# Kernel optimization log

Hardware: AMD Instinct MI355X
Metric: run time of the kernel (lower is better)

The kernel has to match this reference:

```python
import jax, jax.numpy as jnp
import numpy as np

N = 1_000_000
C = 128
B = 16  # number of instances (batch segments)
EPS = 1e-5


def setup_inputs() -> dict:
    key = jax.random.key(0)
    k1, k2 = jax.random.split(key)
    x = jax.random.normal(k1, (N, C), dtype=jnp.float32)
    batch_idx = jnp.sort(jax.random.randint(k2, (N,), 0, B, dtype=jnp.int32))
    weight = jnp.ones((1, C), dtype=jnp.float32)
    bias = jnp.zeros((1, C), dtype=jnp.float32)
    return {"x": x, "batch_idx": batch_idx, "weight": weight, "bias": bias}


def reference(x, batch_idx, weight, bias):
    # per-instance counts [B, 1]
    cnt = jax.ops.segment_sum(jnp.ones((x.shape[0], 1), x.dtype), batch_idx,
                              num_segments=B)
    cnt = jnp.maximum(cnt, 1.0)
    # segment mean [B, C]
    mean = jax.ops.segment_sum(x, batch_idx, num_segments=B) / cnt
    centered = x - mean[batch_idx]               # broadcast-add of -mean
    # segment mean of squared centered features -> per-instance variance [B, C]
    var = jax.ops.segment_sum(centered * centered, batch_idx, num_segments=B) / cnt
    instd = 1.0 / jnp.sqrt(var + EPS)            # [B, C]
    # broadcast-multiply, then affine
    return centered * instd[batch_idx] * weight + bias
```

## Files before the change

### kernel.cpp

```cpp
#include <hip/hip_runtime.h>

#define CC 128
#define BSEG 16
#define EPSV 1e-5f
#define ROWS_PER_BLOCK 512

typedef float v4f __attribute__((ext_vector_type(4)));

__global__ __launch_bounds__(256) void ms_stats(const float* __restrict__ x,
                                                const int* __restrict__ bidx,
                                                int n,
                                                float* __restrict__ sum,
                                                float* __restrict__ sumsq,
                                                float* __restrict__ cnt)
{
    const int r0 = blockIdx.x * ROWS_PER_BLOCK;
    if (r0 >= n) return;
    const int rend = min(r0 + ROWS_PER_BLOCK, n);
    const int tq = threadIdx.x & 31;
    const int tr = threadIdx.x >> 5;

    const int seg_first = bidx[r0];
    const int seg_last  = bidx[rend - 1];

    float s0 = 0.f, s1 = 0.f, s2 = 0.f, s3 = 0.f;
    float q0 = 0.f, q1 = 0.f, q2 = 0.f, q3 = 0.f;

    if (seg_first == seg_last) {
        for (int r = r0 + tr; r < rend; r += 8) {
            const v4f v = *reinterpret_cast<const v4f*>(x + (size_t)r * CC + tq * 4);
            s0 += v.x; s1 += v.y; s2 += v.z; s3 += v.w;
            q0 += v.x * v.x; q1 += v.y * v.y; q2 += v.z * v.z; q3 += v.w * v.w;
        }
        __shared__ float red[8][8][32];
        red[tr][0][tq] = s0; red[tr][1][tq] = s1; red[tr][2][tq] = s2; red[tr][3][tq] = s3;
        red[tr][4][tq] = q0; red[tr][5][tq] = q1; red[tr][6][tq] = q2; red[tr][7][tq] = q3;
        __syncthreads();
        const int j = threadIdx.x >> 5;
        float acc = 0.f;
        #pragma unroll
        for (int k = 0; k < 8; ++k) acc += red[k][j][tq];
        const int ch = tq * 4 + (j & 3);
        atomicAdd(((j < 4) ? sum : sumsq) + seg_first * CC + ch, acc);
        if (threadIdx.x == 0)
            atomicAdd(cnt + seg_first, (float)(rend - r0));
    } else {
        int cur = -1;
        float rows = 0.f;
        for (int r = r0 + tr; r < rend; r += 8) {
            const int seg = bidx[r];
            if (seg != cur) {
                if (cur >= 0) {
                    float* sd = sum   + cur * CC + tq * 4;
                    float* qd = sumsq + cur * CC + tq * 4;
                    atomicAdd(sd + 0, s0); atomicAdd(sd + 1, s1);
                    atomicAdd(sd + 2, s2); atomicAdd(sd + 3, s3);
                    atomicAdd(qd + 0, q0); atomicAdd(qd + 1, q1);
                    atomicAdd(qd + 2, q2); atomicAdd(qd + 3, q3);
                    if (tq == 0) atomicAdd(cnt + cur, rows);
                    s0 = s1 = s2 = s3 = q0 = q1 = q2 = q3 = 0.f;
                    rows = 0.f;
                }
                cur = seg;
            }
            const v4f v = *reinterpret_cast<const v4f*>(x + (size_t)r * CC + tq * 4);
            s0 += v.x; s1 += v.y; s2 += v.z; s3 += v.w;
            q0 += v.x * v.x; q1 += v.y * v.y; q2 += v.z * v.z; q3 += v.w * v.w;
            rows += 1.f;
        }
        if (cur >= 0) {
            float* sd = sum   + cur * CC + tq * 4;
            float* qd = sumsq + cur * CC + tq * 4;
            atomicAdd(sd + 0, s0); atomicAdd(sd + 1, s1);
            atomicAdd(sd + 2, s2); atomicAdd(sd + 3, s3);
            atomicAdd(qd + 0, q0); atomicAdd(qd + 1, q1);
            atomicAdd(qd + 2, q2); atomicAdd(qd + 3, q3);
            if (tq == 0) atomicAdd(cnt + cur, rows);
        }
    }
}

__global__ __launch_bounds__(256) void ms_norm(const float* __restrict__ x,
                                               const int* __restrict__ bidx,
                                               const float* __restrict__ sum,
                                               const float* __restrict__ sumsq,
                                               const float* __restrict__ cnt,
                                               const float* __restrict__ w,
                                               const float* __restrict__ bias,
                                               float* __restrict__ out,
                                               int n)
{
    __shared__ float s_scale[BSEG * CC];
    __shared__ float s_shift[BSEG * CC];
    for (int i = threadIdx.x; i < BSEG * CC; i += 256) {
        const int b = i >> 7;
        const int c = i & (CC - 1);
        const float nn   = fmaxf(cnt[b], 1.0f);
        const float mean = sum[i] / nn;
        const float var  = fmaxf(sumsq[i] / nn - mean * mean, 0.0f);
        const float sc   = rsqrtf(var + EPSV) * w[c];
        s_scale[i] = sc;
        s_shift[i] = fmaf(-mean, sc, bias[c]);
    }
    __syncthreads();

    const unsigned total  = (unsigned)n * 32u;
    const unsigned stride = gridDim.x * blockDim.x;
    for (unsigned i = blockIdx.x * blockDim.x + threadIdx.x; i < total; i += stride) {
        const unsigned idx = total - 1u - i;
        const int r = (int)(idx >> 5);
        const int q = (int)(idx & 31);
        const int seg  = bidx[r];
        const int base = seg * CC + q * 4;
        const v4f v = reinterpret_cast<const v4f*>(x)[idx];
        v4f o;
        o.x = fmaf(v.x, s_scale[base + 0], s_shift[base + 0]);
        o.y = fmaf(v.y, s_scale[base + 1], s_shift[base + 1]);
        o.z = fmaf(v.z, s_scale[base + 2], s_shift[base + 2]);
        o.w = fmaf(v.w, s_scale[base + 3], s_shift[base + 3]);
        __builtin_nontemporal_store(o, reinterpret_cast<v4f*>(out) + idx);
    }
}

extern "C" void kernel_launch(void* const* d_in, const int* in_sizes, int n_in,
                              void* d_out, int out_size, void* d_ws, size_t ws_size,
                              hipStream_t stream)
{
    const float* x    = (const float*)d_in[0];
    const int*   bidx = (const int*)d_in[1];
    const float* w    = (const float*)d_in[2];
    const float* bias = (const float*)d_in[3];
    float* out = (float*)d_out;
    const int n = in_sizes[1];

    float* ws    = (float*)d_ws;
    float* sum   = ws;
    float* sumsq = ws + BSEG * CC;
    float* cnt   = ws + 2 * BSEG * CC;

    (void)hipMemsetAsync(d_ws, 0, (size_t)(2 * BSEG * CC + BSEG) * sizeof(float), stream);

    const int g1 = (n + ROWS_PER_BLOCK - 1) / ROWS_PER_BLOCK;
    ms_stats<<<g1, 256, 0, stream>>>(x, bidx, n, sum, sumsq, cnt);
    ms_norm<<<2048, 256, 0, stream>>>(x, bidx, sum, sumsq, cnt, w, bias, out, n);
}
```

Measured before the change: 316.5 us.

## Process segments in groups so normalize re-reads x from cache

The stats and normalize passes are split into four per-group launches, each covering four consecutive segments (about a quarter of x). The normalize pass re-reads a group's rows soon after the stats pass, so those rows can come from the last-level cache rather than HBM. Segment boundaries are found by binary search on the sorted batch index. That replaces the per-row bidx loads and the count atomics, and the per-row segment lookup becomes comparisons against the boundaries. In exchange there are eight kernel launches instead of two, and the 2048 blocks per launch may be underused on small groups.

```diff
diff --git a/kernel.cpp b/kernel.cpp
--- a/kernel.cpp
+++ b/kernel.cpp
@@ -2,32 +2,52 @@
 
 #define CC 128
 #define BSEG 16
+#define GRP 4
+#define NGRP (BSEG / GRP)
 #define EPSV 1e-5f
-#define ROWS_PER_BLOCK 512
 
 typedef float v4f __attribute__((ext_vector_type(4)));
 
-__global__ __launch_bounds__(256) void ms_stats(const float* __restrict__ x,
-                                                const int* __restrict__ bidx,
-                                                int n,
-                                                float* __restrict__ sum,
-                                                float* __restrict__ sumsq,
-                                                float* __restrict__ cnt)
+__device__ __forceinline__ int lower_bound_dev(const int* __restrict__ a, int n, int v)
 {
-    const int r0 = blockIdx.x * ROWS_PER_BLOCK;
-    if (r0 >= n) return;
-    const int rend = min(r0 + ROWS_PER_BLOCK, n);
+    int lo = 0, hi = n;
+    while (lo < hi) {
+        const int mid = (lo + hi) >> 1;
+        if (a[mid] < v) lo = mid + 1; else hi = mid;
+    }
+    return lo;
+}
+
+__global__ __launch_bounds__(256) void ms_stats_g(const float* __restrict__ x,
+                                                  const int* __restrict__ bidx, int n,
+                                                  float* __restrict__ sum,
+                                                  float* __restrict__ sumsq,
+                                                  int g)
+{
+    __shared__ int sb[GRP + 1];
+    if (threadIdx.x <= GRP)
+        sb[threadIdx.x] = lower_bound_dev(bidx, n, g * GRP + (int)threadIdx.x);
+    __syncthreads();
+    const int b0 = sb[0], b1 = sb[1], b2 = sb[2], b3 = sb[3], b4 = sb[4];
+
+    const int R = b4 - b0;
+    if (R <= 0) return;
+    const int chunk = (R + gridDim.x - 1) / gridDim.x;
+    const int rs = b0 + blockIdx.x * chunk;
+    const int re = min(rs + chunk, b4);
+    if (rs >= re) return;
+
     const int tq = threadIdx.x & 31;
     const int tr = threadIdx.x >> 5;
-
-    const int seg_first = bidx[r0];
-    const int seg_last  = bidx[rend - 1];
 
     float s0 = 0.f, s1 = 0.f, s2 = 0.f, s3 = 0.f;
     float q0 = 0.f, q1 = 0.f, q2 = 0.f, q3 = 0.f;
 
-    if (seg_first == seg_last) {
-        for (int r = r0 + tr; r < rend; r += 8) {
+    const int segA = (rs >= b1) + (rs >= b2) + (rs >= b3);
+    const int segB = ((re - 1) >= b1) + ((re - 1) >= b2) + ((re - 1) >= b3);
+
+    if (segA == segB) {
+        for (int r = rs + tr; r < re; r += 8) {
             const v4f v = *reinterpret_cast<const v4f*>(x + (size_t)r * CC + tq * 4);
             s0 += v.x; s1 += v.y; s2 += v.z; s3 += v.w;
             q0 += v.x * v.x; q1 += v.y * v.y; q2 += v.z * v.z; q3 += v.w * v.w;
@@ -41,83 +61,83 @@
         #pragma unroll
         for (int k = 0; k < 8; ++k) acc += red[k][j][tq];
         const int ch = tq * 4 + (j & 3);
-        atomicAdd(((j < 4) ? sum : sumsq) + seg_first * CC + ch, acc);
-        if (threadIdx.x == 0)
-            atomicAdd(cnt + seg_first, (float)(rend - r0));
+        atomicAdd(((j < 4) ? sum : sumsq) + (g * GRP + segA) * CC + ch, acc);
     } else {
         int cur = -1;
-        float rows = 0.f;
-        for (int r = r0 + tr; r < rend; r += 8) {
-            const int seg = bidx[r];
+        for (int r = rs + tr; r < re; r += 8) {
+            const int seg = (r >= b1) + (r >= b2) + (r >= b3);
             if (seg != cur) {
                 if (cur >= 0) {
-                    float* sd = sum   + cur * CC + tq * 4;
-                    float* qd = sumsq + cur * CC + tq * 4;
+                    float* sd = sum   + (g * GRP + cur) * CC + tq * 4;
+                    float* qd = sumsq + (g * GRP + cur) * CC + tq * 4;
                     atomicAdd(sd + 0, s0); atomicAdd(sd + 1, s1);
                     atomicAdd(sd + 2, s2); atomicAdd(sd + 3, s3);
                     atomicAdd(qd + 0, q0); atomicAdd(qd + 1, q1);
                     atomicAdd(qd + 2, q2); atomicAdd(qd + 3, q3);
-                    if (tq == 0) atomicAdd(cnt + cur, rows);
                     s0 = s1 = s2 = s3 = q0 = q1 = q2 = q3 = 0.f;
-                    rows = 0.f;
                 }
                 cur = seg;
             }
             const v4f v = *reinterpret_cast<const v4f*>(x + (size_t)r * CC + tq * 4);
             s0 += v.x; s1 += v.y; s2 += v.z; s3 += v.w;
             q0 += v.x * v.x; q1 += v.y * v.y; q2 += v.z * v.z; q3 += v.w * v.w;
-            rows += 1.f;
         }
         if (cur >= 0) {
-            float* sd = sum   + cur * CC + tq * 4;
-            float* qd = sumsq + cur * CC + tq * 4;
+            float* sd = sum   + (g * GRP + cur) * CC + tq * 4;
+            float* qd = sumsq + (g * GRP + cur) * CC + tq * 4;
             atomicAdd(sd + 0, s0); atomicAdd(sd + 1, s1);
             atomicAdd(sd + 2, s2); atomicAdd(sd + 3, s3);
             atomicAdd(qd + 0, q0); atomicAdd(qd + 1, q1);
             atomicAdd(qd + 2, q2); atomicAdd(qd + 3, q3);
-            if (tq == 0) atomicAdd(cnt + cur, rows);
         }
     }
 }
 
-__global__ __launch_bounds__(256) void ms_norm(const float* __restrict__ x,
-                                               const int* __restrict__ bidx,
-                                               const float* __restrict__ sum,
-                                               const float* __restrict__ sumsq,
-                                               const float* __restrict__ cnt,
-                                               const float* __restrict__ w,
-                                               const float* __restrict__ bias,
-                                               float* __restrict__ out,
-                                               int n)
+__global__ __launch_bounds__(256) void ms_norm_g(const float* __restrict__ x,
+                                                 const int* __restrict__ bidx, int n,
+                                                 const float* __restrict__ sum,
+                                                 const float* __restrict__ sumsq,
+                                                 const float* __restrict__ w,
+                                                 const float* __restrict__ bias,
+                                                 float* __restrict__ out,
+                                                 int g)
 {
-    __shared__ float s_scale[BSEG * CC];
-    __shared__ float s_shift[BSEG * CC];
-    for (int i = threadIdx.x; i < BSEG * CC; i += 256) {
-        const int b = i >> 7;
-        const int c = i & (CC - 1);
-        const float nn   = fmaxf(cnt[b], 1.0f);
-        const float mean = sum[i] / nn;
-        const float var  = fmaxf(sumsq[i] / nn - mean * mean, 0.0f);
+    __shared__ int sb[GRP + 1];
+    __shared__ v4f s_scale[GRP * 32];
+    __shared__ v4f s_shift[GRP * 32];
+    if (threadIdx.x <= GRP)
+        sb[threadIdx.x] = lower_bound_dev(bidx, n, g * GRP + (int)threadIdx.x);
+    __syncthreads();
+
+    for (int i = threadIdx.x; i < GRP * CC; i += 256) {
+        const int sl = i >> 7;
+        const int c  = i & (CC - 1);
+        const float nn   = fmaxf((float)(sb[sl + 1] - sb[sl]), 1.0f);
+        const int   gi   = (g * GRP + sl) * CC + c;
+        const float mean = sum[gi] / nn;
+        const float var  = fmaxf(sumsq[gi] / nn - mean * mean, 0.0f);
         const float sc   = rsqrtf(var + EPSV) * w[c];
-        s_scale[i] = sc;
-        s_shift[i] = fmaf(-mean, sc, bias[c]);
+        reinterpret_cast<float*>(s_scale)[i] = sc;
+        reinterpret_cast<float*>(s_shift)[i] = fmaf(-mean, sc, bias[c]);
     }
     __syncthreads();
+    const int b1 = sb[1], b2 = sb[2], b3 = sb[3];
 
-    const unsigned total  = (unsigned)n * 32u;
+    const unsigned f0 = (unsigned)sb[0] * 32u;
+    const unsigned f4 = (unsigned)sb[4] * 32u;
     const unsigned stride = gridDim.x * blockDim.x;
-    for (unsigned i = blockIdx.x * blockDim.x + threadIdx.x; i < total; i += stride) {
-        const unsigned idx = total - 1u - i;
-        const int r = (int)(idx >> 5);
-        const int q = (int)(idx & 31);
-        const int seg  = bidx[r];
-        const int base = seg * CC + q * 4;
-        const v4f v = reinterpret_cast<const v4f*>(x)[idx];
+    for (unsigned idx = f0 + blockIdx.x * blockDim.x + threadIdx.x; idx < f4; idx += stride) {
+        const int r  = (int)(idx >> 5);
+        const int q  = (int)(idx & 31);
+        const int sl = (r >= b1) + (r >= b2) + (r >= b3);
+        const v4f v  = reinterpret_cast<const v4f*>(x)[idx];
+        const v4f sc = s_scale[sl * 32 + q];
+        const v4f sh = s_shift[sl * 32 + q];
         v4f o;
-        o.x = fmaf(v.x, s_scale[base + 0], s_shift[base + 0]);
-        o.y = fmaf(v.y, s_scale[base + 1], s_shift[base + 1]);
-        o.z = fmaf(v.z, s_scale[base + 2], s_shift[base + 2]);
-        o.w = fmaf(v.w, s_scale[base + 3], s_shift[base + 3]);
+        o.x = fmaf(v.x, sc.x, sh.x);
+        o.y = fmaf(v.y, sc.y, sh.y);
+        o.z = fmaf(v.z, sc.z, sh.z);
+        o.w = fmaf(v.w, sc.w, sh.w);
         __builtin_nontemporal_store(o, reinterpret_cast<v4f*>(out) + idx);
     }
 }
@@ -136,11 +156,11 @@
     float* ws    = (float*)d_ws;
     float* sum   = ws;
     float* sumsq = ws + BSEG * CC;
-    float* cnt   = ws + 2 * BSEG * CC;
 
-    (void)hipMemsetAsync(d_ws, 0, (size_t)(2 * BSEG * CC + BSEG) * sizeof(float), stream);
+    (void)hipMemsetAsync(d_ws, 0, (size_t)(2 * BSEG * CC) * sizeof(float), stream);
 
-    const int g1 = (n + ROWS_PER_BLOCK - 1) / ROWS_PER_BLOCK;
-    ms_stats<<<g1, 256, 0, stream>>>(x, bidx, n, sum, sumsq, cnt);
-    ms_norm<<<2048, 256, 0, stream>>>(x, bidx, sum, sumsq, cnt, w, bias, out, n);
+    for (int g = 0; g < NGRP; ++g) {
+        ms_stats_g<<<2048, 256, 0, stream>>>(x, bidx, n, sum, sumsq, g);
+        ms_norm_g<<<2048, 256, 0, stream>>>(x, bidx, n, sum, sumsq, w, bias, out, g);
+    }
 }
```

Result: slower. 408.4 us (+29.0%).

## Restructure norm kernel into contiguous per-block chunks with register-cached per-segment scale

Applied to the files above, without the earlier changes.

The normalize kernel no longer builds a shared-memory scale/shift table for all segments in every block. Each block now walks a contiguous chunk backwards in 8-float pairs, and each thread keeps a fixed channel group. The thread recomputes scale and shift in registers only when the segment changes. This removes the per-block table setup, the barrier and the LDS lookups, at the cost of 8-wide accesses whose stride between lanes may coalesce less well. The stats kernel also unrolls its uniform-segment loop by two, using vector accumulators.

```diff
diff --git a/kernel.cpp b/kernel.cpp
--- a/kernel.cpp
+++ b/kernel.cpp
@@ -4,8 +4,20 @@
 #define BSEG 16
 #define EPSV 1e-5f
 #define ROWS_PER_BLOCK 512
+#define NORM_GRID 2048
 
 typedef float v4f __attribute__((ext_vector_type(4)));
+
+__device__ __forceinline__ v4f vmax0(v4f a)
+{
+    v4f r; r.x = fmaxf(a.x, 0.f); r.y = fmaxf(a.y, 0.f);
+    r.z = fmaxf(a.z, 0.f); r.w = fmaxf(a.w, 0.f); return r;
+}
+__device__ __forceinline__ v4f vrsqrt_eps(v4f a)
+{
+    v4f r; r.x = rsqrtf(a.x + EPSV); r.y = rsqrtf(a.y + EPSV);
+    r.z = rsqrtf(a.z + EPSV); r.w = rsqrtf(a.w + EPSV); return r;
+}
 
 __global__ __launch_bounds__(256) void ms_stats(const float* __restrict__ x,
                                                 const int* __restrict__ bidx,
@@ -23,18 +35,24 @@
     const int seg_first = bidx[r0];
     const int seg_last  = bidx[rend - 1];
 
-    float s0 = 0.f, s1 = 0.f, s2 = 0.f, s3 = 0.f;
-    float q0 = 0.f, q1 = 0.f, q2 = 0.f, q3 = 0.f;
+    v4f s = {0.f, 0.f, 0.f, 0.f};
+    v4f q = {0.f, 0.f, 0.f, 0.f};
 
     if (seg_first == seg_last) {
-        for (int r = r0 + tr; r < rend; r += 8) {
-            const v4f v = *reinterpret_cast<const v4f*>(x + (size_t)r * CC + tq * 4);
-            s0 += v.x; s1 += v.y; s2 += v.z; s3 += v.w;
-            q0 += v.x * v.x; q1 += v.y * v.y; q2 += v.z * v.z; q3 += v.w * v.w;
+        int r = r0 + tr;
+        for (; r + 8 < rend; r += 16) {
+            const v4f a = *reinterpret_cast<const v4f*>(x + (size_t)r * CC + tq * 4);
+            const v4f b = *reinterpret_cast<const v4f*>(x + (size_t)(r + 8) * CC + tq * 4);
+            s += a; q += a * a;
+            s += b; q += b * b;
+        }
+        if (r < rend) {
+            const v4f a = *reinterpret_cast<const v4f*>(x + (size_t)r * CC + tq * 4);
+            s += a; q += a * a;
         }
         __shared__ float red[8][8][32];
-        red[tr][0][tq] = s0; red[tr][1][tq] = s1; red[tr][2][tq] = s2; red[tr][3][tq] = s3;
-        red[tr][4][tq] = q0; red[tr][5][tq] = q1; red[tr][6][tq] = q2; red[tr][7][tq] = q3;
+        red[tr][0][tq] = s.x; red[tr][1][tq] = s.y; red[tr][2][tq] = s.z; red[tr][3][tq] = s.w;
+        red[tr][4][tq] = q.x; red[tr][5][tq] = q.y; red[tr][6][tq] = q.z; red[tr][7][tq] = q.w;
         __syncthreads();
         const int j = threadIdx.x >> 5;
         float acc = 0.f;
@@ -53,28 +71,28 @@
                 if (cur >= 0) {
                     float* sd = sum   + cur * CC + tq * 4;
                     float* qd = sumsq + cur * CC + tq * 4;
-                    atomicAdd(sd + 0, s0); atomicAdd(sd + 1, s1);
-                    atomicAdd(sd + 2, s2); atomicAdd(sd + 3, s3);
-                    atomicAdd(qd + 0, q0); atomicAdd(qd + 1, q1);
-                    atomicAdd(qd + 2, q2); atomicAdd(qd + 3, q3);
+                    atomicAdd(sd + 0, s.x); atomicAdd(sd + 1, s.y);
+                    atomicAdd(sd + 2, s.z); atomicAdd(sd + 3, s.w);
+                    atomicAdd(qd + 0, q.x); atomicAdd(qd + 1, q.y);
+                    atomicAdd(qd + 2, q.z); atomicAdd(qd + 3, q.w);
                     if (tq == 0) atomicAdd(cnt + cur, rows);
-                    s0 = s1 = s2 = s3 = q0 = q1 = q2 = q3 = 0.f;
+                    s = (v4f){0.f, 0.f, 0.f, 0.f};
+                    q = (v4f){0.f, 0.f, 0.f, 0.f};
                     rows = 0.f;
                 }
                 cur = seg;
             }
-            const v4f v = *reinterpret_cast<const v4f*>(x + (size_t)r * CC + tq * 4);
-            s0 += v.x; s1 += v.y; s2 += v.z; s3 += v.w;
-            q0 += v.x * v.x; q1 += v.y * v.y; q2 += v.z * v.z; q3 += v.w * v.w;
+            const v4f a = *reinterpret_cast<const v4f*>(x + (size_t)r * CC + tq * 4);
+            s += a; q += a * a;
             rows += 1.f;
         }
         if (cur >= 0) {
             float* sd = sum   + cur * CC + tq * 4;
             float* qd = sumsq + cur * CC + tq * 4;
-            atomicAdd(sd + 0, s0); atomicAdd(sd + 1, s1);
-            atomicAdd(sd + 2, s2); atomicAdd(sd + 3, s3);
-            atomicAdd(qd + 0, q0); atomicAdd(qd + 1, q1);
-            atomicAdd(qd + 2, q2); atomicAdd(qd + 3, q3);
+            atomicAdd(sd + 0, s.x); atomicAdd(sd + 1, s.y);
+            atomicAdd(sd + 2, s.z); atomicAdd(sd + 3, s.w);
+            atomicAdd(qd + 0, q.x); atomicAdd(qd + 1, q.y);
+            atomicAdd(qd + 2, q.z); atomicAdd(qd + 3, q.w);
             if (tq == 0) atomicAdd(cnt + cur, rows);
         }
     }
@@ -90,35 +108,51 @@
                                                float* __restrict__ out,
                                                int n)
 {
-    __shared__ float s_scale[BSEG * CC];
-    __shared__ float s_shift[BSEG * CC];
-    for (int i = threadIdx.x; i < BSEG * CC; i += 256) {
-        const int b = i >> 7;
-        const int c = i & (CC - 1);
-        const float nn   = fmaxf(cnt[b], 1.0f);
-        const float mean = sum[i] / nn;
-        const float var  = fmaxf(sumsq[i] / nn - mean * mean, 0.0f);
-        const float sc   = rsqrtf(var + EPSV) * w[c];
-        s_scale[i] = sc;
-        s_shift[i] = fmaf(-mean, sc, bias[c]);
-    }
-    __syncthreads();
+    const int npairs = n * 16;
+    const int chunk  = (npairs + (int)gridDim.x - 1) / (int)gridDim.x;
+    const int hi     = npairs - (int)blockIdx.x * chunk;
+    if (hi <= 0) return;
+    const int lo     = max(hi - chunk, 0);
+    const int tid    = (int)threadIdx.x;
 
-    const unsigned total  = (unsigned)n * 32u;
-    const unsigned stride = gridDim.x * blockDim.x;
-    for (unsigned i = blockIdx.x * blockDim.x + threadIdx.x; i < total; i += stride) {
-        const unsigned idx = total - 1u - i;
-        const int r = (int)(idx >> 5);
-        const int q = (int)(idx & 31);
-        const int seg  = bidx[r];
-        const int base = seg * CC + q * 4;
-        const v4f v = reinterpret_cast<const v4f*>(x)[idx];
-        v4f o;
-        o.x = fmaf(v.x, s_scale[base + 0], s_shift[base + 0]);
-        o.y = fmaf(v.y, s_scale[base + 1], s_shift[base + 1]);
-        o.z = fmaf(v.z, s_scale[base + 2], s_shift[base + 2]);
-        o.w = fmaf(v.w, s_scale[base + 3], s_shift[base + 3]);
-        __builtin_nontemporal_store(o, reinterpret_cast<v4f*>(out) + idx);
+    const int c0 = ((hi + tid) & 15) * 8;
+    const v4f w0 = *reinterpret_cast<const v4f*>(w + c0);
+    const v4f w1 = *reinterpret_cast<const v4f*>(w + c0 + 4);
+    const v4f b0 = *reinterpret_cast<const v4f*>(bias + c0);
+    const v4f b1 = *reinterpret_cast<const v4f*>(bias + c0 + 4);
+
+    int cur = -1;
+    v4f sc0, sc1, sh0, sh1;
+
+    for (int p = hi - 256 + tid; p >= lo; p -= 256) {
+        const int r   = p >> 4;
+        const int seg = bidx[r];
+        if (seg != cur) {
+            cur = seg;
+            const int gi  = seg * CC + c0;
+            const v4f su0 = *reinterpret_cast<const v4f*>(sum + gi);
+            const v4f su1 = *reinterpret_cast<const v4f*>(sum + gi + 4);
+            const v4f sq0 = *reinterpret_cast<const v4f*>(sumsq + gi);
+            const v4f sq1 = *reinterpret_cast<const v4f*>(sumsq + gi + 4);
+            const float rn = 1.0f / fmaxf(cnt[seg], 1.0f);
+            const v4f m0 = su0 * rn;
+            const v4f m1 = su1 * rn;
+            const v4f is0 = vrsqrt_eps(vmax0(sq0 * rn - m0 * m0));
+            const v4f is1 = vrsqrt_eps(vmax0(sq1 * rn - m1 * m1));
+            sc0 = is0 * w0; sc1 = is1 * w1;
+            sh0 = b0 - m0 * sc0; sh1 = b1 - m1 * sc1;
+        }
+        const float* px = x + (size_t)p * 8;
+        const v4f a = *reinterpret_cast<const v4f*>(px);
+        const v4f b = *reinterpret_cast<const v4f*>(px + 4);
+        v4f o0, o1;
+        o0.x = fmaf(a.x, sc0.x, sh0.x); o0.y = fmaf(a.y, sc0.y, sh0.y);
+        o0.z = fmaf(a.z, sc0.z, sh0.z); o0.w = fmaf(a.w, sc0.w, sh0.w);
+        o1.x = fmaf(b.x, sc1.x, sh1.x); o1.y = fmaf(b.y, sc1.y, sh1.y);
+        o1.z = fmaf(b.z, sc1.z, sh1.z); o1.w = fmaf(b.w, sc1.w, sh1.w);
+        float* po = out + (size_t)p * 8;
+        __builtin_nontemporal_store(o0, reinterpret_cast<v4f*>(po));
+        __builtin_nontemporal_store(o1, reinterpret_cast<v4f*>(po + 4));
     }
 }
 
@@ -142,5 +176,5 @@
 
     const int g1 = (n + ROWS_PER_BLOCK - 1) / ROWS_PER_BLOCK;
     ms_stats<<<g1, 256, 0, stream>>>(x, bidx, n, sum, sumsq, cnt);
-    ms_norm<<<2048, 256, 0, stream>>>(x, bidx, sum, sumsq, cnt, w, bias, out, n);
+    ms_norm<<<NORM_GRID, 256, 0, stream>>>(x, bidx, sum, sumsq, cnt, w, bias, out, n);
 }
```

Result: slower. 345.2 us (+9.1%).
